# Kernel optimization log

Hardware: AMD Instinct MI355X
Metric: run time of the kernel (lower is better)

Reference implementation:

```python
import jax, jax.numpy as jnp
import numpy as np

N_ATOMS = 4096
K = 24                 # exact neighbors per atom (regular neighbor list)
RC = 6.0

# sf_spec parameters (see init_kwargs)
G2_RS = jnp.array([0.5, 2.0, 3.5, 5.0], jnp.float32)
G2_ETA = jnp.array([4.0, 4.0, 4.0, 4.0], jnp.float32)
G4_LAMBD = jnp.array([1.0, 1.0, -1.0, -1.0], jnp.float32)
G4_ZETA = jnp.array([1.0, 4.0, 1.0, 4.0], jnp.float32)
G4_ETA = jnp.array([0.01, 0.05, 0.01, 0.05], jnp.float32)


def setup_inputs() -> dict:
    key = jax.random.key(0)
    k1, k2, k3, k4 = jax.random.split(key, 4)
    n_pairs = N_ATOMS * K
    i_ind = jnp.repeat(jnp.arange(N_ATOMS, dtype=jnp.int32), K)
    off = jax.random.randint(k1, (n_pairs,), 1, N_ATOMS, dtype=jnp.int32)
    j_ind = (i_ind + off) % N_ATOMS
    ind_2 = jnp.stack([i_ind, j_ind], axis=1)          # [n_pairs,2], sorted by i
    dirs = jax.random.normal(k2, (n_pairs, 3), jnp.float32)
    dirs = dirs / jnp.linalg.norm(dirs, axis=1, keepdims=True)
    r = jax.random.uniform(k3, (n_pairs,), jnp.float32, 0.8, RC - 0.1)
    diff = dirs * r[:, None]                           # [n_pairs,3], |diff| < rc
    elems = jax.random.randint(k4, (N_ATOMS,), 1, 4, dtype=jnp.int32)
    return {"ind_2": ind_2, "elems": elems, "diff": diff}


def fc_f1(dist):
    # CutoffFunc 'f1': 0.5*(cos(pi*r/rc)+1)
    return 0.5 * (jnp.cos(jnp.pi * dist / RC) + 1.0)


def form_triplet(ind_2, n_atoms):
    """Faithful _form_triplet; triplet count is static because every atom has
    exactly K = n_pairs//n_atoms neighbors."""
    n_pairs = ind_2.shape[0]
    Kn = n_pairs // n_atoms
    p_iind = ind_2[:, 0]
    p_aind = jnp.arange(1, n_pairs + 1, dtype=jnp.int32)         # cumsum(ones)
    seg_min = jax.ops.segment_min(p_aind, p_iind, num_segments=n_atoms)
    p_rind = p_aind - seg_min[p_iind]                            # rank within group
    t_dense = jnp.zeros((n_atoms, Kn), jnp.int32).at[p_iind, p_rind].set(p_aind)
    t_dense = t_dense[p_iind]                                    # [n_pairs, K]
    t_ijind = jnp.repeat(jnp.arange(n_pairs, dtype=jnp.int32), Kn)
    t_ikind = t_dense.reshape(-1) - 1                            # row-major like tf.where
    keep = jnp.nonzero(t_ijind != t_ikind, size=n_pairs * (Kn - 1))[0]
    return jnp.stack([t_ijind[keep], t_ikind[keep]], axis=1)


def g2_fp(dist, fc, i_ind, n_atoms):
    # G2_SF with i=j='ALL'
    sf = jnp.exp(-G2_ETA * (dist[:, None] - G2_RS) ** 2) * fc[:, None]
    return jax.ops.segment_sum(sf, i_ind, num_segments=n_atoms)


def g4_fp(dist, fc, diff, ind_2, ind_3, n_atoms):
    # G4_SF with i=j=k='ALL' (Behler G5-style, no jk cutoff)
    ij, ik = ind_3[:, 0], ind_3[:, 1]
    i_rind = ind_2[:, 0][ij]
    d_ij, d_ik = diff[ij], diff[ik]
    R_ij, R_ik = dist[ij], dist[ik]
    fc_ij, fc_ik = fc[ij], fc[ik]
    cos = jnp.sum(d_ij * d_ik, axis=1) / (R_ij * R_ik)
    sf = (2.0 ** (1.0 - G4_ZETA)
          * (1.0 + G4_LAMBD * cos[:, None]) ** G4_ZETA
          * jnp.exp(-G4_ETA * (R_ij ** 2 + R_ik ** 2)[:, None])
          * (fc_ij * fc_ik)[:, None])
    return jax.ops.segment_sum(sf, i_rind, num_segments=n_atoms)


def reference(ind_2, elems, diff):
    n_atoms = elems.shape[0]
    n_pairs = ind_2.shape[0]
    ind_3 = form_triplet(ind_2, n_atoms)
    i_ind = ind_2[:, 0]

    def fps_fn(d):
        # connect_dist_grad: dist recomputed from diff so grads flow
        dist = jnp.linalg.norm(d, axis=1)
        fc = fc_f1(dist)
        fp0 = g2_fp(dist, fc, i_ind, n_atoms)
        fp1 = g4_fp(dist, fc, d, ind_2, ind_3, n_atoms)
        return fp0, fp1

    fp0, fp1 = fps_fn(diff)
    # Per-column Jacobian wrt diff (each pair row feeds exactly one atom, so
    # grad of column-sum equals the per-row Jacobian entries)
    jac0, jac1 = jax.jacrev(lambda d: tuple(f.sum(0) for f in fps_fn(d)))(diff)
    jacob0 = jnp.transpose(jac0, (1, 2, 0))   # [n_pairs, 3, n_g2]
    jacob1 = jnp.transpose(jac1, (1, 2, 0))   # [n_pairs, 3, n_g4]
    p_ind = jnp.arange(n_pairs, dtype=jnp.int32)
    jacob_ind = jnp.stack([p_ind, i_ind], axis=1)  # [pair, center-atom]
    return fp0, jacob0, jacob_ind, fp1, jacob1, jacob_ind
```

## Files before the change

kernel.cpp:

```cpp
#include <hip/hip_runtime.h>

#define NA   4096
#define KN   24
#define NP   (NA*KN)
#define APB  8
#define PPB  (APB*KN)
#define NS   4
#define TPB  (NS*PPB)

#define OFF_J0   (NA*4)
#define OFF_JI   (OFF_J0 + NP*12)
#define OFF_FP1  (OFF_JI + NP*2)
#define OFF_J1   (OFF_FP1 + NA*4)
#define OFF_JI2  (OFF_J1 + NP*12)


__global__ __launch_bounds__(TPB) void bpsf_kernel(const float* __restrict__ diff,
                                                   float* __restrict__ out)
{
    const int t = threadIdx.x;
    const int s = t / PPB;
    const int u = t - s * PPB;
    const int aloc = u / KN;
    const int r = u - aloc * KN;
    const int atom = blockIdx.x * APB + aloc;
    const int p = atom * KN + r;

    __shared__ float4 s_pd[PPB];
    __shared__ float  s_w2[PPB];
    __shared__ float2 s_g[PPB];
    __shared__ float  s_sf0[PPB][5];
    __shared__ float  s_sf1[PPB][5];
    __shared__ float  s_part[3*PPB][21];

    float R=0.f, invR=0.f;

    if (s == 0) {
        const float dx = diff[3*p+0];
        const float dy = diff[3*p+1];
        const float dz = diff[3*p+2];
        const float Rsq = dx*dx + dy*dy + dz*dz;
        R    = sqrtf(Rsq);
        invR = __builtin_amdgcn_rcpf(R);
        float sn, cs;
        __sincosf(0.52359877559829887f * R, &sn, &cs);
        const float fc  = 0.5f * (cs + 1.0f);
        const float fcp = -0.26179938779914943f * sn;
        const float E1  = __expf(-0.01f * Rsq);
        const float e1s = E1 * E1;
        const float E2  = e1s * e1s * E1;

        s_pd[u] = make_float4(dx*invR, dy*invR, dz*invR, fc*E1);
        s_w2[u] = fc * E2;
        s_g[u]  = make_float2(fcp*E1, fcp*E2);
    } else if (s == 1) {
        const float dx = diff[3*p+0];
        const float dy = diff[3*p+1];
        const float dz = diff[3*p+2];
        const float Rsq = dx*dx + dy*dy + dz*dz;
        const float Rl    = sqrtf(Rsq);
        const float invRl = __builtin_amdgcn_rcpf(Rl);
        float sn, cs;
        __sincosf(0.52359877559829887f * Rl, &sn, &cs);
        const float fc  = 0.5f * (cs + 1.0f);
        const float fcp = -0.26179938779914943f * sn;

        const float rs[4] = {0.5f, 2.0f, 3.5f, 5.0f};
        float j0[12];
        #pragma unroll
        for (int m = 0; m < 4; ++m) {
            const float dr = Rl - rs[m];
            const float g  = __expf(-4.0f * dr * dr);
            s_sf0[u][m] = g * fc;
            const float coef = invRl * g * (fcp - 8.0f * dr * fc);
            j0[0*4+m] = dx * coef;
            j0[1*4+m] = dy * coef;
            j0[2*4+m] = dz * coef;
        }
        float4* o = (float4*)(out + OFF_J0 + p * 12);
        o[0] = make_float4(j0[0], j0[1], j0[2],  j0[3]);
        o[1] = make_float4(j0[4], j0[5], j0[6],  j0[7]);
        o[2] = make_float4(j0[8], j0[9], j0[10], j0[11]);
    } else if (s == 2) {
        const float2 ji = make_float2((float)p, (float)atom);
        *(float2*)(out + OFF_JI  + 2*p) = ji;
        *(float2*)(out + OFF_JI2 + 2*p) = ji;
    }

    __syncthreads();

    const float4 pr = s_pd[u];
    const float ux = pr.x, uy = pr.y, uz = pr.z;
    const float W1p = pr.w;
    const float W2p = s_w2[u];
    const float2 gg = s_g[u];
    const float G1p = gg.x, G2p = gg.y;

    float V1x=0,V1y=0,V1z=0, V2x=0,V2y=0,V2z=0, V3x=0,V3y=0,V3z=0;
    float S1=0,S2=0,S3=0, QH1=0,QcH1=0,Q1=0,Q3=0;
    float F0=0,F1=0,F2=0,F3=0;

    const int qbase = aloc * KN;

    #pragma unroll
    for (int k = 0; k < KN/NS; ++k) {
        const int qr = NS*k + s;
        const int q  = qbase + qr;
        const float4 qd = s_pd[q];
        const bool self = (qr == r);
        const float W1q = self ? 0.0f : qd.w;
        const float W2q = self ? 0.0f : s_w2[q];
        const float qx = qd.x, qy = qd.y, qz = qd.z;

        const float c   = ux*qx + uy*qy + uz*qz;
        const float P1  = W1p * W1q;
        const float P2  = W2p * W2q;
        const float H1  = G1p * W1q;
        const float H2  = G2p * W2q;

        const float cP1 = c * P1;
        F0 += P1 + cP1;
        F2 += P1 - cP1;
        S1 += cP1;
        QH1  += H1;
        QcH1 += c * H1;
        V1x += P1*qx; V1y += P1*qy; V1z += P1*qz;

        const float bp  = 1.0f + c, bm = 1.0f - c;
        const float bp2 = bp*bp,    bm2 = bm*bm;
        const float bp4 = bp2*bp2,  bm4 = bm2*bm2;
        const float A1  = 0.125f * bp4;
        const float A3  = 0.125f * bm4;
        const float d1h = bp2 * bp;
        const float d3h = bm2 * bm;
        const float a1  = P2 * d1h;
        const float a3  = P2 * d3h;
        F1 += A1 * P2;
        F3 += A3 * P2;
        S2 += a1 * c;
        S3 += a3 * c;
        Q1 += A1 * H2;
        Q3 += A3 * H2;
        V2x += a1*qx; V2y += a1*qy; V2z += a1*qz;
        V3x += a3*qx; V3y += a3*qy; V3z += a3*qz;
    }

    if (s) {
        float* w = s_part[(s-1)*PPB + u];
        w[0]=V1x; w[1]=V1y; w[2]=V1z; w[3]=V2x; w[4]=V2y; w[5]=V2z;
        w[6]=V3x; w[7]=V3y; w[8]=V3z; w[9]=S1; w[10]=S2; w[11]=S3;
        w[12]=QH1; w[13]=QcH1; w[14]=Q1; w[15]=Q3;
        w[16]=F0; w[17]=F1; w[18]=F2; w[19]=F3;
    }
    __syncthreads();

    if (s == 0) {
        #pragma unroll
        for (int g = 0; g < 3; ++g) {
            const float* w = s_part[g*PPB + u];
            V1x+=w[0]; V1y+=w[1]; V1z+=w[2]; V2x+=w[3]; V2y+=w[4]; V2z+=w[5];
            V3x+=w[6]; V3y+=w[7]; V3z+=w[8]; S1+=w[9]; S2+=w[10]; S3+=w[11];
            QH1+=w[12]; QcH1+=w[13]; Q1+=w[14]; Q3+=w[15];
            F0+=w[16]; F1+=w[17]; F2+=w[18]; F3+=w[19];
        }

        const float iR  = invR;
        const float iRh = 0.5f * invR;
        const float t0 = -0.02f * R * F0 + (QH1 + QcH1);
        const float t2 = -0.02f * R * F2 + (QH1 - QcH1);
        const float t1 = -0.10f * R * F1 + Q1;
        const float t3 = -0.10f * R * F3 + Q3;

        const float a0x = iR *(V1x - S1*ux) + t0*ux;
        const float a0y = iR *(V1y - S1*uy) + t0*uy;
        const float a0z = iR *(V1z - S1*uz) + t0*uz;
        const float a1x = iRh*(V2x - S2*ux) + t1*ux;
        const float a1y = iRh*(V2y - S2*uy) + t1*uy;
        const float a1z = iRh*(V2z - S2*uz) + t1*uz;
        const float a2x = -iR *(V1x - S1*ux) + t2*ux;
        const float a2y = -iR *(V1y - S1*uy) + t2*uy;
        const float a2z = -iR *(V1z - S1*uz) + t2*uz;
        const float a3x = -iRh*(V3x - S3*ux) + t3*ux;
        const float a3y = -iRh*(V3y - S3*uy) + t3*uy;
        const float a3z = -iRh*(V3z - S3*uz) + t3*uz;

        float4* o = (float4*)(out + OFF_J1 + p * 12);
        o[0] = make_float4(2.0f*a0x, 2.0f*a1x, 2.0f*a2x, 2.0f*a3x);
        o[1] = make_float4(2.0f*a0y, 2.0f*a1y, 2.0f*a2y, 2.0f*a3y);
        o[2] = make_float4(2.0f*a0z, 2.0f*a1z, 2.0f*a2z, 2.0f*a3z);

        s_sf1[u][0]=F0; s_sf1[u][1]=F1; s_sf1[u][2]=F2; s_sf1[u][3]=F3;
    }
    __syncthreads();

    if (t < APB * 4) {
        const int a2 = t >> 2;
        const int m  = t & 3;
        const int src = a2 * KN;
        float s0 = 0.0f, s1 = 0.0f;
        for (int rr = 0; rr < KN; ++rr) {
            s0 += s_sf0[src + rr][m];
            s1 += s_sf1[src + rr][m];
        }
        const int ga = blockIdx.x * APB + a2;
        out[ga * 4 + m]           = s0;
        out[OFF_FP1 + ga * 4 + m] = s1;
    }
}

extern "C" void kernel_launch(void* const* d_in, const int* in_sizes, int n_in,
                              void* d_out, int out_size, void* d_ws, size_t ws_size,
                              hipStream_t stream) {
    const float* diff = (const float*)d_in[2];
    float* out = (float*)d_out;
    bpsf_kernel<<<NA / APB, TPB, 0, stream>>>(diff, out);
}
```

Before: 12.36 us.

## Overlap fingerprint reduction with Jacobian epilogue and use nontemporal stores

Removes the final __syncthreads by having slice-1 threads reduce the G2 and G4 fingerprints directly from the partial-sum buffers while slice-0 threads compute and write the G4 Jacobian. The G4 fingerprint is summed over all four slices' partial F values, so nothing has to wait for the s0 reduction. All global output writes now use nontemporal stores to avoid cache pollution, and a shared subexpression in the Jacobian epilogue is computed once. This adds more shared-memory reads per reduction thread and may cause bank conflicts on the stride-21 partial buffer.

```diff
diff --git a/kernel.cpp b/kernel.cpp
--- a/kernel.cpp
+++ b/kernel.cpp
@@ -13,6 +13,18 @@
 #define OFF_FP1  (OFF_JI + NP*2)
 #define OFF_J1   (OFF_FP1 + NA*4)
 #define OFF_JI2  (OFF_J1 + NP*12)
+
+typedef float f32x4 __attribute__((ext_vector_type(4)));
+typedef float f32x2 __attribute__((ext_vector_type(2)));
+
+__device__ __forceinline__ void nt_store4(float* p, float a, float b, float c, float d) {
+    f32x4 v = {a, b, c, d};
+    __builtin_nontemporal_store(v, (f32x4*)p);
+}
+__device__ __forceinline__ void nt_store2(float* p, float a, float b) {
+    f32x2 v = {a, b};
+    __builtin_nontemporal_store(v, (f32x2*)p);
+}
 
 
 __global__ __launch_bounds__(TPB) void bpsf_kernel(const float* __restrict__ diff,
@@ -30,7 +42,7 @@
     __shared__ float  s_w2[PPB];
     __shared__ float2 s_g[PPB];
     __shared__ float  s_sf0[PPB][5];
-    __shared__ float  s_sf1[PPB][5];
+    __shared__ float  s_f0g[PPB][4];
     __shared__ float  s_part[3*PPB][21];
 
     float R=0.f, invR=0.f;
@@ -77,14 +89,13 @@
             j0[1*4+m] = dy * coef;
             j0[2*4+m] = dz * coef;
         }
-        float4* o = (float4*)(out + OFF_J0 + p * 12);
-        o[0] = make_float4(j0[0], j0[1], j0[2],  j0[3]);
-        o[1] = make_float4(j0[4], j0[5], j0[6],  j0[7]);
-        o[2] = make_float4(j0[8], j0[9], j0[10], j0[11]);
+        float* o = out + OFF_J0 + p * 12;
+        nt_store4(o+0, j0[0], j0[1], j0[2],  j0[3]);
+        nt_store4(o+4, j0[4], j0[5], j0[6],  j0[7]);
+        nt_store4(o+8, j0[8], j0[9], j0[10], j0[11]);
     } else if (s == 2) {
-        const float2 ji = make_float2((float)p, (float)atom);
-        *(float2*)(out + OFF_JI  + 2*p) = ji;
-        *(float2*)(out + OFF_JI2 + 2*p) = ji;
+        nt_store2(out + OFF_JI  + 2*p, (float)p, (float)atom);
+        nt_store2(out + OFF_JI2 + 2*p, (float)p, (float)atom);
     }
 
     __syncthreads();
@@ -151,6 +162,8 @@
         w[6]=V3x; w[7]=V3y; w[8]=V3z; w[9]=S1; w[10]=S2; w[11]=S3;
         w[12]=QH1; w[13]=QcH1; w[14]=Q1; w[15]=Q3;
         w[16]=F0; w[17]=F1; w[18]=F2; w[19]=F3;
+    } else {
+        s_f0g[u][0]=F0; s_f0g[u][1]=F1; s_f0g[u][2]=F2; s_f0g[u][3]=F3;
     }
     __syncthreads();
 
@@ -171,40 +184,42 @@
         const float t1 = -0.10f * R * F1 + Q1;
         const float t3 = -0.10f * R * F3 + Q3;
 
-        const float a0x = iR *(V1x - S1*ux) + t0*ux;
-        const float a0y = iR *(V1y - S1*uy) + t0*uy;
-        const float a0z = iR *(V1z - S1*uz) + t0*uz;
+        const float b1x = iR *(V1x - S1*ux), b1y = iR *(V1y - S1*uy), b1z = iR *(V1z - S1*uz);
+        const float a0x =  b1x + t0*ux, a0y =  b1y + t0*uy, a0z =  b1z + t0*uz;
+        const float a2x = -b1x + t2*ux, a2y = -b1y + t2*uy, a2z = -b1z + t2*uz;
         const float a1x = iRh*(V2x - S2*ux) + t1*ux;
         const float a1y = iRh*(V2y - S2*uy) + t1*uy;
         const float a1z = iRh*(V2z - S2*uz) + t1*uz;
-        const float a2x = -iR *(V1x - S1*ux) + t2*ux;
-        const float a2y = -iR *(V1y - S1*uy) + t2*uy;
-        const float a2z = -iR *(V1z - S1*uz) + t2*uz;
         const float a3x = -iRh*(V3x - S3*ux) + t3*ux;
         const float a3y = -iRh*(V3y - S3*uy) + t3*uy;
         const float a3z = -iRh*(V3z - S3*uz) + t3*uz;
 
-        float4* o = (float4*)(out + OFF_J1 + p * 12);
-        o[0] = make_float4(2.0f*a0x, 2.0f*a1x, 2.0f*a2x, 2.0f*a3x);
-        o[1] = make_float4(2.0f*a0y, 2.0f*a1y, 2.0f*a2y, 2.0f*a3y);
-        o[2] = make_float4(2.0f*a0z, 2.0f*a1z, 2.0f*a2z, 2.0f*a3z);
-
-        s_sf1[u][0]=F0; s_sf1[u][1]=F1; s_sf1[u][2]=F2; s_sf1[u][3]=F3;
-    }
-    __syncthreads();
-
-    if (t < APB * 4) {
-        const int a2 = t >> 2;
-        const int m  = t & 3;
+        float* o = out + OFF_J1 + p * 12;
+        nt_store4(o+0, 2.0f*a0x, 2.0f*a1x, 2.0f*a2x, 2.0f*a3x);
+        nt_store4(o+4, 2.0f*a0y, 2.0f*a1y, 2.0f*a2y, 2.0f*a3y);
+        nt_store4(o+8, 2.0f*a0z, 2.0f*a1z, 2.0f*a2z, 2.0f*a3z);
+    } else if (s == 1 && u < 2 * APB * 4) {
+        const bool g4 = (u < APB * 4);
+        const int v  = g4 ? u : u - APB * 4;
+        const int a2 = v >> 2;
+        const int m  = v & 3;
         const int src = a2 * KN;
-        float s0 = 0.0f, s1 = 0.0f;
-        for (int rr = 0; rr < KN; ++rr) {
-            s0 += s_sf0[src + rr][m];
-            s1 += s_sf1[src + rr][m];
+        float acc = 0.0f;
+        if (g4) {
+            #pragma unroll
+            for (int rr = 0; rr < KN; ++rr) {
+                const int slot = src + rr;
+                acc += s_f0g[slot][m]
+                     + s_part[0*PPB + slot][16+m]
+                     + s_part[1*PPB + slot][16+m]
+                     + s_part[2*PPB + slot][16+m];
+            }
+        } else {
+            #pragma unroll
+            for (int rr = 0; rr < KN; ++rr) acc += s_sf0[src + rr][m];
         }
         const int ga = blockIdx.x * APB + a2;
-        out[ga * 4 + m]           = s0;
-        out[OFF_FP1 + ga * 4 + m] = s1;
+        __builtin_nontemporal_store(acc, out + (g4 ? OFF_FP1 : 0) + ga * 4 + m);
     }
 }
 
```

Result: no change. 12.12 us (-2.0%).
